# Kernel optimization log

Measured on AMD Instinct MI355X. Metric: run time of the kernel, lower is better.

Reference implementation:

```python
import jax, jax.numpy as jnp
import numpy as np

N_NODES = 100000
N_EDGES = 1600000
IN_CH = 128
HID = 128   # 2 * out_channels
OUT_CH = 64


def setup_inputs() -> dict:
    key = jax.random.key(0)
    k1, k2, k3, k4, k5, k6 = jax.random.split(key, 6)
    x = jax.random.normal(k1, (N_NODES, IN_CH), dtype=jnp.float32)
    edge_index = jax.random.randint(k2, (2, N_EDGES), 0, N_NODES, dtype=jnp.int64)
    W1 = jax.random.normal(k3, (IN_CH, HID), dtype=jnp.float32) / np.sqrt(IN_CH)
    b1 = jax.random.normal(k4, (HID,), dtype=jnp.float32) * 0.01
    W2 = jax.random.normal(k5, (HID, OUT_CH), dtype=jnp.float32) / np.sqrt(HID)
    b2 = jax.random.normal(k6, (OUT_CH,), dtype=jnp.float32) * 0.01
    return {"x": x, "edge_index": edge_index, "W1": W1, "b1": b1, "W2": W2, "b2": b2}


def _gcn_layer(x, src, dst, norm, W, b, n_nodes):
    # GCNConv: linear transform, then normalized scatter-add aggregation + bias
    h = x @ W                                   # [N, d_out]
    msg = h[src] * norm[:, None]                # gather + edge normalize, [E+N, d_out]
    out = jax.ops.segment_sum(msg, dst, num_segments=n_nodes)
    return out + b


def reference(x, edge_index, W1, b1, W2, b2):
    n = x.shape[0]
    loop = jnp.arange(n, dtype=edge_index.dtype)
    # add self-loops (PyG GCNConv default)
    src = jnp.concatenate([edge_index[0], loop])
    dst = jnp.concatenate([edge_index[1], loop])
    # symmetric normalization deg^-1/2[src] * deg^-1/2[dst]
    deg = jax.ops.segment_sum(jnp.ones_like(dst, x.dtype), dst, num_segments=n)
    dinv = jnp.where(deg > 0, jax.lax.rsqrt(deg), 0.0)
    norm = dinv[src] * dinv[dst]

    h = jax.nn.relu(_gcn_layer(x, src, dst, norm, W1, b1, n))
    out = jax.nn.relu(_gcn_layer(h, src, dst, norm, W2, b2, n))
    return out
```

## Files before the change

### kernel.cpp

```cpp
#include <hip/hip_runtime.h>
#include <hip/hip_fp16.h>

typedef _Float16 f16x8 __attribute__((ext_vector_type(8)));
typedef float f32x4 __attribute__((ext_vector_type(4)));

#define BSH 9
#define BSZ 512
#define CAP 12288

__global__ __launch_bounds__(256) void passA(const int* __restrict__ ei,
                                             int* __restrict__ bcount, int E, int NB) {
  __shared__ int hist[256];
  int t = threadIdx.x;
  hist[t] = 0;
  __syncthreads();
  for (int e = blockIdx.x * 256 + t; e < E; e += gridDim.x * 256)
    atomicAdd(&hist[ei[E + e] >> BSH], 1);
  __syncthreads();
  if (t < NB && hist[t]) atomicAdd(&bcount[t], hist[t]);
}

__global__ __launch_bounds__(256) void scanB(const int* __restrict__ bcount,
                                             int* __restrict__ bstart,
                                             int* __restrict__ bfill, int NB, int E) {
  __shared__ int s[256];
  int t = threadIdx.x;
  int v = (t < NB) ? bcount[t] : 0;
  s[t] = v;
  __syncthreads();
  for (int off = 1; off < 256; off <<= 1) {
    int add = (t >= off) ? s[t - off] : 0;
    __syncthreads();
    s[t] += add;
    __syncthreads();
  }
  if (t < NB) {
    int ex = s[t] - v;
    bstart[t] = ex;
    bfill[t] = ex;
  }
  if (t == 0) bstart[NB] = E;
}

template <int NC, int NWC, bool IN_F16, bool SCALE>
__device__ __forceinline__ void gemm_mfma_body(
    const void* __restrict__ Xv, const float* __restrict__ W,
    const float* __restrict__ dinv, _Float16* __restrict__ G, int nrows, int bid,
    _Float16* Bs) {
  int t = threadIdx.x;
  {
    int n = t % NC;
    int kh = (t / NC) * (NC / 2);
    constexpr int NBLK = (NC / 2) / 8;
#pragma unroll
    for (int b = 0; b < NBLK; ++b) {
      f16x8 tmp;
#pragma unroll
      for (int j = 0; j < 8; ++j)
        tmp[j] = (_Float16)W[(size_t)(kh + b * 8 + j) * NC + n];
      *(f16x8*)(&Bs[n * 136 + kh + b * 8]) = tmp;
    }
  }
  __syncthreads();

  int w = t >> 6, lane = t & 63;
  int m = lane & 15, q = lane >> 4;
  int wr = (w / NWC) * 64, wc = (w % NWC) * 64;
  int row0 = bid * ((4 / NWC) * 64);

  f32x4 acc[4][4];
#pragma unroll
  for (int rt = 0; rt < 4; ++rt)
#pragma unroll
    for (int ct = 0; ct < 4; ++ct)
#pragma unroll
      for (int qq = 0; qq < 4; ++qq) acc[rt][ct][qq] = 0.f;

#pragma unroll
  for (int kc = 0; kc < 4; ++kc) {
    int kbase = kc * 32 + q * 8;
    f16x8 af[4];
#pragma unroll
    for (int rt = 0; rt < 4; ++rt) {
      int row = row0 + wr + rt * 16 + m;
      if constexpr (IN_F16) {
        f16x8 a = {0, 0, 0, 0, 0, 0, 0, 0};
        if (row < nrows) a = *(const f16x8*)((const _Float16*)Xv + (size_t)row * 128 + kbase);
        af[rt] = a;
      } else {
        float4 x0 = {0, 0, 0, 0}, x1 = {0, 0, 0, 0};
        if (row < nrows) {
          const float* Xf = (const float*)Xv;
          x0 = *(const float4*)(Xf + (size_t)row * 128 + kbase);
          x1 = *(const float4*)(Xf + (size_t)row * 128 + kbase + 4);
        }
        f16x8 a;
        a[0] = (_Float16)x0.x; a[1] = (_Float16)x0.y;
        a[2] = (_Float16)x0.z; a[3] = (_Float16)x0.w;
        a[4] = (_Float16)x1.x; a[5] = (_Float16)x1.y;
        a[6] = (_Float16)x1.z; a[7] = (_Float16)x1.w;
        af[rt] = a;
      }
    }
    f16x8 bf[4];
#pragma unroll
    for (int ct = 0; ct < 4; ++ct) {
      int n = wc + ct * 16 + m;
      bf[ct] = *(f16x8*)(&Bs[n * 136 + kbase]);
    }
#pragma unroll
    for (int rt = 0; rt < 4; ++rt)
#pragma unroll
      for (int ct = 0; ct < 4; ++ct)
        acc[rt][ct] = __builtin_amdgcn_mfma_f32_16x16x32_f16(af[rt], bf[ct],
                                                             acc[rt][ct], 0, 0, 0);
  }
#pragma unroll
  for (int rt = 0; rt < 4; ++rt) {
#pragma unroll
    for (int r = 0; r < 4; ++r) {
      int row = row0 + wr + rt * 16 + q * 4 + r;
      if (row < nrows) {
        float d = SCALE ? dinv[row] : 1.f;
#pragma unroll
        for (int ct = 0; ct < 4; ++ct) {
          int col = wc + ct * 16 + m;
          G[(size_t)row * NC + col] = (_Float16)(acc[rt][ct][r] * d);
        }
      }
    }
  }
}

__global__ __launch_bounds__(256) void fused_gemm_passB(
    const float* __restrict__ X, const float* __restrict__ W1,
    _Float16* __restrict__ G, int nrows, int GB,
    const int* __restrict__ ei, int* __restrict__ bfill,
    unsigned int* __restrict__ pairs, int E, int PB) {
  __shared__ char smem[128 * 136 * 2];
  int g = blockIdx.x;
  int M2 = 2 * (GB < PB ? GB : PB);
  bool is_gemm;
  int bid;
  if (g < M2) { is_gemm = (g & 1) == 0; bid = g >> 1; }
  else        { is_gemm = (GB > PB);    bid = g - M2 + (GB < PB ? GB : PB); }
  if (is_gemm) {
    gemm_mfma_body<128, 2, false, false>(X, W1, nullptr, G, nrows, bid,
                                         (_Float16*)smem);
  } else {
    int* hist = (int*)smem;
    int* gbase = (int*)(smem + 1024);
    int t = threadIdx.x;
    hist[t] = 0;
    __syncthreads();
    int d[8], s[8], lp[8], bb[8];
    int base = bid * 2048;
#pragma unroll
    for (int u = 0; u < 8; ++u) {
      int e = base + u * 256 + t;
      if (e < E) {
        d[u] = ei[E + e];
        s[u] = ei[e];
        bb[u] = d[u] >> BSH;
        lp[u] = atomicAdd(&hist[bb[u]], 1);
      } else {
        bb[u] = -1;
      }
    }
    __syncthreads();
    if (hist[t]) gbase[t] = atomicAdd(&bfill[t], hist[t]);
    __syncthreads();
#pragma unroll
    for (int u = 0; u < 8; ++u)
      if (bb[u] >= 0)
        pairs[gbase[bb[u]] + lp[u]] =
            ((unsigned int)(d[u] & (BSZ - 1)) << 17) | (unsigned int)s[u];
  }
}

__global__ __launch_bounds__(256) void gemm2_mfma(const _Float16* __restrict__ X,
                                                  const float* __restrict__ W,
                                                  const float* __restrict__ dinv,
                                                  _Float16* __restrict__ G, int nrows) {
  __shared__ _Float16 Bs[64 * 136];
  gemm_mfma_body<64, 1, true, true>(X, W, dinv, G, nrows, blockIdx.x, Bs);
}

__global__ __launch_bounds__(512) void passC(const unsigned int* __restrict__ pairs,
                                             const int* __restrict__ bstart,
                                             int* __restrict__ rowstart,
                                             int* __restrict__ deg,
                                             float* __restrict__ dinv,
                                             int* __restrict__ csr, int N) {
  __shared__ int hcnt[BSZ];
  __shared__ int lfill[BSZ];
  __shared__ int ss[512];
  __shared__ int lcsr[CAP];
  int b = blockIdx.x;
  int t = threadIdx.x;
  int lo = bstart[b], hi = bstart[b + 1];
  int cnt = hi - lo;
  int nbase = b << BSH;
  hcnt[t] = 0;
  __syncthreads();
  for (int k = lo + t; k < hi; k += 512)
    atomicAdd(&hcnt[(pairs[k] >> 17) & (BSZ - 1)], 1);
  __syncthreads();
  int v = hcnt[t];
  ss[t] = v;
  __syncthreads();
  for (int off = 1; off < 512; off <<= 1) {
    int add = (t >= off) ? ss[t - off] : 0;
    __syncthreads();
    ss[t] += add;
    __syncthreads();
  }
  int ex = ss[t] - v;
  lfill[t] = ex;
  int node = nbase + t;
  if (node < N) {
    rowstart[node] = lo + ex;
    deg[node] = v;
    dinv[node] = rsqrtf((float)(v + 1));
  }
  __syncthreads();
  bool fits = (cnt <= CAP);
  for (int k = lo + t; k < hi; k += 512) {
    unsigned int p = pairs[k];
    int pos = atomicAdd(&lfill[(p >> 17) & (BSZ - 1)], 1);
    int src = (int)(p & 0x1FFFFu);
    if (fits) lcsr[pos] = src;
    else      csr[lo + pos] = src;
  }
  __syncthreads();
  if (fits)
    for (int k = t; k < cnt; k += 512) csr[lo + k] = lcsr[k];
}

__global__ __launch_bounds__(256) void agg128(
    const __half* __restrict__ G, const int* __restrict__ csr,
    const int* __restrict__ rowstart, const int* __restrict__ deg,
    const float* __restrict__ dinv, const float* __restrict__ bias,
    __half* __restrict__ out, int n) {
  int wid = blockIdx.x * 4 + (threadIdx.x >> 6);
  if (wid >= n) return;
  int i = __builtin_amdgcn_readfirstlane(wid);
  int lane = threadIdx.x & 63;
  const __half2* Gp = (const __half2*)G;
  float di = dinv[i];
  float2 g = __half22float2(Gp[(size_t)i * 64 + lane]);
  float2 a = {di * g.x, di * g.y};
  int s = rowstart[i];
  int d = deg[i];
  int cnt = d < 64 ? d : 64;
  int myidx = 0;
  if (lane < cnt) myidx = csr[s + lane];
  int k = 0;
  for (; k + 3 < cnt; k += 4) {
    int s0 = __builtin_amdgcn_readfirstlane(__shfl(myidx, k));
    int s1 = __builtin_amdgcn_readfirstlane(__shfl(myidx, k + 1));
    int s2 = __builtin_amdgcn_readfirstlane(__shfl(myidx, k + 2));
    int s3 = __builtin_amdgcn_readfirstlane(__shfl(myidx, k + 3));
    float w0 = dinv[s0], w1 = dinv[s1], w2 = dinv[s2], w3 = dinv[s3];
    float2 v0 = __half22float2(Gp[(size_t)s0 * 64 + lane]);
    float2 v1 = __half22float2(Gp[(size_t)s1 * 64 + lane]);
    float2 v2 = __half22float2(Gp[(size_t)s2 * 64 + lane]);
    float2 v3 = __half22float2(Gp[(size_t)s3 * 64 + lane]);
    a.x = fmaf(w0, v0.x, a.x); a.y = fmaf(w0, v0.y, a.y);
    a.x = fmaf(w1, v1.x, a.x); a.y = fmaf(w1, v1.y, a.y);
    a.x = fmaf(w2, v2.x, a.x); a.y = fmaf(w2, v2.y, a.y);
    a.x = fmaf(w3, v3.x, a.x); a.y = fmaf(w3, v3.y, a.y);
  }
  for (; k < cnt; ++k) {
    int s0 = __builtin_amdgcn_readfirstlane(__shfl(myidx, k));
    float w0 = dinv[s0];
    float2 v0 = __half22float2(Gp[(size_t)s0 * 64 + lane]);
    a.x = fmaf(w0, v0.x, a.x); a.y = fmaf(w0, v0.y, a.y);
  }
  for (int j = s + 64; j < s + d; ++j) {
    int s0 = __builtin_amdgcn_readfirstlane(csr[j]);
    float w0 = dinv[s0];
    float2 v0 = __half22float2(Gp[(size_t)s0 * 64 + lane]);
    a.x = fmaf(w0, v0.x, a.x); a.y = fmaf(w0, v0.y, a.y);
  }
  float2 b = ((const float2*)bias)[lane];
  float ox = fmaxf(fmaf(di, a.x, b.x), 0.f);
  float oy = fmaxf(fmaf(di, a.y, b.y), 0.f);
  ((__half2*)out)[(size_t)i * 64 + lane] = __floats2half2_rn(ox, oy);
}

__global__ __launch_bounds__(256) void agg64(
    const __half* __restrict__ G, const int* __restrict__ csr,
    const int* __restrict__ rowstart, const int* __restrict__ deg,
    const float* __restrict__ dinv, const float* __restrict__ bias,
    float* __restrict__ out, int n) {
  int wid = blockIdx.x * 4 + (threadIdx.x >> 6);
  if (wid >= n) return;
  int i = __builtin_amdgcn_readfirstlane(wid);
  int lane = threadIdx.x & 63;
  float a = __half2float(G[(size_t)i * 64 + lane]);
  int s = rowstart[i];
  int d = deg[i];
  int cnt = d < 64 ? d : 64;
  int myidx = 0;
  if (lane < cnt) myidx = csr[s + lane];
  int k = 0;
  for (; k + 3 < cnt; k += 4) {
    int s0 = __builtin_amdgcn_readfirstlane(__shfl(myidx, k));
    int s1 = __builtin_amdgcn_readfirstlane(__shfl(myidx, k + 1));
    int s2 = __builtin_amdgcn_readfirstlane(__shfl(myidx, k + 2));
    int s3 = __builtin_amdgcn_readfirstlane(__shfl(myidx, k + 3));
    float v0 = __half2float(G[(size_t)s0 * 64 + lane]);
    float v1 = __half2float(G[(size_t)s1 * 64 + lane]);
    float v2 = __half2float(G[(size_t)s2 * 64 + lane]);
    float v3 = __half2float(G[(size_t)s3 * 64 + lane]);
    a += (v0 + v1) + (v2 + v3);
  }
  for (; k < cnt; ++k) {
    int s0 = __builtin_amdgcn_readfirstlane(__shfl(myidx, k));
    a += __half2float(G[(size_t)s0 * 64 + lane]);
  }
  for (int j = s + 64; j < s + d; ++j) {
    int s0 = __builtin_amdgcn_readfirstlane(csr[j]);
    a += __half2float(G[(size_t)s0 * 64 + lane]);
  }
  float o = fmaxf(fmaf(dinv[i], a, bias[lane]), 0.f);
  out[(size_t)i * 64 + lane] = o;
}

extern "C" void kernel_launch(void* const* d_in, const int* in_sizes, int n_in,
                              void* d_out, int out_size, void* d_ws, size_t ws_size,
                              hipStream_t stream) {
  const float* x  = (const float*)d_in[0];
  const int*   ei = (const int*)d_in[1];
  const float* W1 = (const float*)d_in[2];
  const float* b1 = (const float*)d_in[3];
  const float* W2 = (const float*)d_in[4];
  const float* b2 = (const float*)d_in[5];
  float* out = (float*)d_out;

  const int N = in_sizes[0] / 128;
  const int E = in_sizes[1] / 2;
  const int NB = (N + BSZ - 1) >> BSH;

  char* base = (char*)d_ws;
  size_t off = 0;
  auto alloc = [&](size_t bytes) -> void* {
    void* p = base + off;
    off += (bytes + 255) & ~(size_t)255;
    return p;
  };
  int*          bcount   = (int*)alloc(256 * 4);
  int*          bstart   = (int*)alloc(260 * 4);
  int*          bfill    = (int*)alloc(256 * 4);
  int*          deg      = (int*)alloc((size_t)N * 4);
  int*          rowstart = (int*)alloc((size_t)N * 4);
  float*        dinv     = (float*)alloc((size_t)N * 4);
  int*          csr      = (int*)alloc((size_t)E * 4);
  unsigned int* pairs    = (unsigned int*)alloc((size_t)E * 4);
  __half*       g1       = (__half*)alloc((size_t)N * 128 * 2);
  __half*       x2       = (__half*)alloc((size_t)N * 128 * 2);

  hipMemsetAsync(bcount, 0, 256 * 4, stream);
  passA<<<512, 256, 0, stream>>>(ei, bcount, E, NB);
  scanB<<<1, 256, 0, stream>>>(bcount, bstart, bfill, NB, E);

  int GB = (N + 127) / 128;
  int PB = (E + 2047) / 2048;
  fused_gemm_passB<<<GB + PB, 256, 0, stream>>>(x, W1, (_Float16*)g1, N, GB, ei,
                                                bfill, pairs, E, PB);
  passC<<<NB, 512, 0, stream>>>(pairs, bstart, rowstart, deg, dinv, csr, N);

  agg128<<<(N + 3) / 4, 256, 0, stream>>>(g1, csr, rowstart, deg, dinv, b1, x2, N);
  int G2B = (N + 255) / 256;
  gemm2_mfma<<<G2B, 256, 0, stream>>>((const _Float16*)x2, W2, dinv,
                                      (_Float16*)g1, N);
  agg64<<<(N + 3) / 4, 256, 0, stream>>>(g1, csr, rowstart, deg, dinv, b2, out, N);
}
```

Measured before the change: 296.9 us.

## Split each wavefront into four edge groups with 16-byte vector row gathers

Both aggregation kernels now split a 64-lane wavefront into four groups of 16 lanes. Each group gathers a different neighbor row with wide f16x8/f16x4 loads, so four to eight edges are in flight per iteration. The partial sums are then reduced across groups with xor shuffles. The aim is fewer, wider memory requests and more gather parallelism for each node. The cost is reduction shuffles, masked padding lanes that gather the self row, and only a quarter of the lanes writing the output.

```diff
diff --git a/kernel.cpp b/kernel.cpp
--- a/kernel.cpp
+++ b/kernel.cpp
@@ -2,6 +2,7 @@
 #include <hip/hip_fp16.h>
 
 typedef _Float16 f16x8 __attribute__((ext_vector_type(8)));
+typedef _Float16 f16x4 __attribute__((ext_vector_type(4)));
 typedef float f32x4 __attribute__((ext_vector_type(4)));
 
 #define BSH 9
@@ -246,47 +247,56 @@
   if (wid >= n) return;
   int i = __builtin_amdgcn_readfirstlane(wid);
   int lane = threadIdx.x & 63;
-  const __half2* Gp = (const __half2*)G;
+  int g = lane >> 4;
+  int c = lane & 15;
+  const _Float16* Gh = (const _Float16*)G;
   float di = dinv[i];
-  float2 g = __half22float2(Gp[(size_t)i * 64 + lane]);
-  float2 a = {di * g.x, di * g.y};
+  f16x8 self = *(const f16x8*)(Gh + (size_t)i * 128 + c * 8);
+  float wself = (g == 0) ? di : 0.f;
+  float a[8];
+#pragma unroll
+  for (int j = 0; j < 8; ++j) a[j] = wself * (float)self[j];
   int s = rowstart[i];
   int d = deg[i];
-  int cnt = d < 64 ? d : 64;
-  int myidx = 0;
-  if (lane < cnt) myidx = csr[s + lane];
-  int k = 0;
-  for (; k + 3 < cnt; k += 4) {
-    int s0 = __builtin_amdgcn_readfirstlane(__shfl(myidx, k));
-    int s1 = __builtin_amdgcn_readfirstlane(__shfl(myidx, k + 1));
-    int s2 = __builtin_amdgcn_readfirstlane(__shfl(myidx, k + 2));
-    int s3 = __builtin_amdgcn_readfirstlane(__shfl(myidx, k + 3));
-    float w0 = dinv[s0], w1 = dinv[s1], w2 = dinv[s2], w3 = dinv[s3];
-    float2 v0 = __half22float2(Gp[(size_t)s0 * 64 + lane]);
-    float2 v1 = __half22float2(Gp[(size_t)s1 * 64 + lane]);
-    float2 v2 = __half22float2(Gp[(size_t)s2 * 64 + lane]);
-    float2 v3 = __half22float2(Gp[(size_t)s3 * 64 + lane]);
-    a.x = fmaf(w0, v0.x, a.x); a.y = fmaf(w0, v0.y, a.y);
-    a.x = fmaf(w1, v1.x, a.x); a.y = fmaf(w1, v1.y, a.y);
-    a.x = fmaf(w2, v2.x, a.x); a.y = fmaf(w2, v2.y, a.y);
-    a.x = fmaf(w3, v3.x, a.x); a.y = fmaf(w3, v3.y, a.y);
-  }
-  for (; k < cnt; ++k) {
-    int s0 = __builtin_amdgcn_readfirstlane(__shfl(myidx, k));
-    float w0 = dinv[s0];
-    float2 v0 = __half22float2(Gp[(size_t)s0 * 64 + lane]);
-    a.x = fmaf(w0, v0.x, a.x); a.y = fmaf(w0, v0.y, a.y);
-  }
-  for (int j = s + 64; j < s + d; ++j) {
-    int s0 = __builtin_amdgcn_readfirstlane(csr[j]);
-    float w0 = dinv[s0];
-    float2 v0 = __half22float2(Gp[(size_t)s0 * 64 + lane]);
-    a.x = fmaf(w0, v0.x, a.x); a.y = fmaf(w0, v0.y, a.y);
-  }
-  float2 b = ((const float2*)bias)[lane];
-  float ox = fmaxf(fmaf(di, a.x, b.x), 0.f);
-  float oy = fmaxf(fmaf(di, a.y, b.y), 0.f);
-  ((__half2*)out)[(size_t)i * 64 + lane] = __floats2half2_rn(ox, oy);
+  for (int base = 0; base < d; base += 64) {
+    int chunk = d - base;
+    if (chunk > 64) chunk = 64;
+    int myidx = (lane < chunk) ? csr[s + base + lane] : i;
+    for (int k = 0; k < chunk; k += 8) {
+      int sl0 = k + g, sl1 = k + 4 + g;
+      int s0 = __shfl(myidx, sl0);
+      int s1 = __shfl(myidx, sl1);
+      float w0 = dinv[s0];
+      float w1 = dinv[s1];
+      if (sl0 >= chunk) w0 = 0.f;
+      if (sl1 >= chunk) w1 = 0.f;
+      f16x8 v0 = *(const f16x8*)(Gh + (size_t)s0 * 128 + c * 8);
+      f16x8 v1 = *(const f16x8*)(Gh + (size_t)s1 * 128 + c * 8);
+#pragma unroll
+      for (int j = 0; j < 8; ++j) a[j] = fmaf(w0, (float)v0[j], a[j]);
+#pragma unroll
+      for (int j = 0; j < 8; ++j) a[j] = fmaf(w1, (float)v1[j], a[j]);
+    }
+  }
+#pragma unroll
+  for (int j = 0; j < 8; ++j) {
+    a[j] += __shfl_xor(a[j], 16);
+    a[j] += __shfl_xor(a[j], 32);
+  }
+  if (g == 0) {
+    float4 b0 = *(const float4*)(bias + c * 8);
+    float4 b1 = *(const float4*)(bias + c * 8 + 4);
+    f16x8 r;
+    r[0] = (_Float16)fmaxf(fmaf(di, a[0], b0.x), 0.f);
+    r[1] = (_Float16)fmaxf(fmaf(di, a[1], b0.y), 0.f);
+    r[2] = (_Float16)fmaxf(fmaf(di, a[2], b0.z), 0.f);
+    r[3] = (_Float16)fmaxf(fmaf(di, a[3], b0.w), 0.f);
+    r[4] = (_Float16)fmaxf(fmaf(di, a[4], b1.x), 0.f);
+    r[5] = (_Float16)fmaxf(fmaf(di, a[5], b1.y), 0.f);
+    r[6] = (_Float16)fmaxf(fmaf(di, a[6], b1.z), 0.f);
+    r[7] = (_Float16)fmaxf(fmaf(di, a[7], b1.w), 0.f);
+    *(f16x8*)((_Float16*)out + (size_t)i * 128 + c * 8) = r;
+  }
 }
 
 __global__ __launch_bounds__(256) void agg64(
@@ -298,34 +308,49 @@
   if (wid >= n) return;
   int i = __builtin_amdgcn_readfirstlane(wid);
   int lane = threadIdx.x & 63;
-  float a = __half2float(G[(size_t)i * 64 + lane]);
+  int g = lane >> 4;
+  int c = lane & 15;
+  const _Float16* Gh = (const _Float16*)G;
+  f16x4 self = *(const f16x4*)(Gh + (size_t)i * 64 + c * 4);
+  float wself = (g == 0) ? 1.f : 0.f;
+  float a[4];
+#pragma unroll
+  for (int j = 0; j < 4; ++j) a[j] = wself * (float)self[j];
   int s = rowstart[i];
   int d = deg[i];
-  int cnt = d < 64 ? d : 64;
-  int myidx = 0;
-  if (lane < cnt) myidx = csr[s + lane];
-  int k = 0;
-  for (; k + 3 < cnt; k += 4) {
-    int s0 = __builtin_amdgcn_readfirstlane(__shfl(myidx, k));
-    int s1 = __builtin_amdgcn_readfirstlane(__shfl(myidx, k + 1));
-    int s2 = __builtin_amdgcn_readfirstlane(__shfl(myidx, k + 2));
-    int s3 = __builtin_amdgcn_readfirstlane(__shfl(myidx, k + 3));
-    float v0 = __half2float(G[(size_t)s0 * 64 + lane]);
-    float v1 = __half2float(G[(size_t)s1 * 64 + lane]);
-    float v2 = __half2float(G[(size_t)s2 * 64 + lane]);
-    float v3 = __half2float(G[(size_t)s3 * 64 + lane]);
-    a += (v0 + v1) + (v2 + v3);
-  }
-  for (; k < cnt; ++k) {
-    int s0 = __builtin_amdgcn_readfirstlane(__shfl(myidx, k));
-    a += __half2float(G[(size_t)s0 * 64 + lane]);
-  }
-  for (int j = s + 64; j < s + d; ++j) {
-    int s0 = __builtin_amdgcn_readfirstlane(csr[j]);
-    a += __half2float(G[(size_t)s0 * 64 + lane]);
-  }
-  float o = fmaxf(fmaf(dinv[i], a, bias[lane]), 0.f);
-  out[(size_t)i * 64 + lane] = o;
+  for (int base = 0; base < d; base += 64) {
+    int chunk = d - base;
+    if (chunk > 64) chunk = 64;
+    int myidx = (lane < chunk) ? csr[s + base + lane] : i;
+    for (int k = 0; k < chunk; k += 8) {
+      int sl0 = k + g, sl1 = k + 4 + g;
+      int s0 = __shfl(myidx, sl0);
+      int s1 = __shfl(myidx, sl1);
+      float w0 = (sl0 < chunk) ? 1.f : 0.f;
+      float w1 = (sl1 < chunk) ? 1.f : 0.f;
+      f16x4 v0 = *(const f16x4*)(Gh + (size_t)s0 * 64 + c * 4);
+      f16x4 v1 = *(const f16x4*)(Gh + (size_t)s1 * 64 + c * 4);
+#pragma unroll
+      for (int j = 0; j < 4; ++j) a[j] = fmaf(w0, (float)v0[j], a[j]);
+#pragma unroll
+      for (int j = 0; j < 4; ++j) a[j] = fmaf(w1, (float)v1[j], a[j]);
+    }
+  }
+#pragma unroll
+  for (int j = 0; j < 4; ++j) {
+    a[j] += __shfl_xor(a[j], 16);
+    a[j] += __shfl_xor(a[j], 32);
+  }
+  if (g == 0) {
+    float di = dinv[i];
+    float4 bv = *(const float4*)(bias + c * 4);
+    float4 r;
+    r.x = fmaxf(fmaf(di, a[0], bv.x), 0.f);
+    r.y = fmaxf(fmaf(di, a[1], bv.y), 0.f);
+    r.z = fmaxf(fmaf(di, a[2], bv.z), 0.f);
+    r.w = fmaxf(fmaf(di, a[3], bv.w), 0.f);
+    *(float4*)(out + (size_t)i * 64 + c * 4) = r;
+  }
 }
 
 extern "C" void kernel_launch(void* const* d_in, const int* in_sizes, int n_in,
```

After: 282.4 us. 1.05x faster.
